# Kernel optimization log

Measured on AMD Instinct MI355X. Metric: run time of the kernel, lower is better.

The kernel has to match this reference:

```python
import jax, jax.numpy as jnp
import numpy as np

B, N, E, H, L, T, IN = 32, 512, 32768, 64, 2, 2, 8
TAU = 0.5


def setup_inputs() -> dict:
    key = jax.random.key(0)
    ks = jax.random.split(key, 32)
    f = lambda i, shape, s=0.05: jax.random.normal(ks[i], shape, jnp.float32) * s
    u = jax.random.uniform(ks[3], (B, E, T), jnp.float32, 1e-6, 1.0 - 1e-6)
    return {
        "inputs": f(0, (B, N, IN), 1.0),
        "hidden": f(1, (B, N, H), 1.0),
        "edge_logits": f(2, (B, E, T), 1.0),
        "gumbel": -jnp.log(-jnp.log(u)),  # standard Gumbel noise (deterministic here)
        "send_edges": jax.random.randint(ks[4], (E,), 0, N),
        "recv_edges": jax.random.randint(ks[5], (E,), 0, N),
        "W1": f(6, (L, T, H, 2 * H)), "b1": f(7, (L, T, H)),
        "W2": f(8, (L, T, H, H)), "b2": f(9, (L, T, H)),
        "Whr": f(10, (H, L * H)), "Whi": f(11, (H, L * H)), "Whh": f(12, (H, L * H)),
        "Wir": f(13, (H, IN)), "bir": f(14, (H,)),
        "Wii": f(15, (H, IN)), "bii": f(16, (H,)),
        "Win": f(17, (H, IN)), "bin_w": f(18, (H,)),
        "Wm1": f(19, (H, H)), "bm1": f(20, (H,)),
        "Wm2": f(21, (H, H)), "bm2": f(22, (H,)),
        "Wdf": f(23, (N, N * H), 0.005), "bdf": f(24, (N,)),
        "Wloc": f(25, (N, N * H), 0.005), "bloc": f(26, (N,)),
        "Wscale": f(27, (N, N * H), 0.005), "bscale": f(28, (N,)),
    }


def _lin(x, W, b):
    return jnp.einsum('...i,oi->...o', x, W) + b


def reference(inputs, hidden, edge_logits, gumbel, send_edges, recv_edges,
              W1, b1, W2, b2, Whr, Whi, Whh,
              Wir, bir, Wii, bii, Win, bin_w,
              Wm1, bm1, Wm2, bm2,
              Wdf, bdf, Wloc, bloc, Wscale, bscale):
    # hard gumbel-softmax (straight-through)
    y_soft = jax.nn.softmax((edge_logits + gumbel) / TAU, axis=-1)
    y_hard = jax.nn.one_hot(jnp.argmax(y_soft, axis=-1), T, dtype=y_soft.dtype)
    edges = jax.lax.stop_gradient(y_hard - y_soft) + y_soft  # [B,E,T]

    # normalized receiver degree (zeros -> 1), as in edge2node_mat / degree
    deg = jnp.zeros((N,), jnp.float32).at[recv_edges].add(1.0)
    deg = jnp.where(deg == 0, 1.0, deg)

    hidden_ = hidden
    aggs = []
    norm = float(T)  # skip_first_edge_type=False
    for k in range(L):
        pre = jnp.concatenate([hidden_[:, recv_edges], hidden_[:, send_edges]], axis=-1)  # [B,E,2H]
        all_msgs = jnp.zeros((B, E, H), pre.dtype)
        for t in range(T):  # per-edge-type tanh MLP (eval mode: dropout off)
            m = jnp.tanh(jnp.einsum('bef,hf->beh', pre, W1[k, t]) + b1[k, t])
            m = jnp.tanh(jnp.einsum('beh,gh->beg', m, W2[k, t]) + b2[k, t])
            all_msgs = all_msgs + m * edges[:, :, t:t + 1] / norm
        # scatter-mean onto receiver nodes (= normalized edge2node matmul)
        agg = jnp.zeros((B, N, H), all_msgs.dtype).at[:, recv_edges].add(all_msgs) / deg[None, :, None]
        hidden_ = agg
        aggs.append(agg)
    agg = jnp.concatenate(aggs, axis=-1)  # [B,N,L*H]

    r = jax.nn.sigmoid(_lin(inputs, Wir, bir) + jnp.einsum('bnf,of->bno', agg, Whr))
    i = jax.nn.sigmoid(_lin(inputs, Wii, bii) + jnp.einsum('bnf,of->bno', agg, Whi))
    n = jnp.tanh(_lin(inputs, Win, bin_w) + r * jnp.einsum('bnf,of->bno', agg, Whh))
    hidden_new = (1.0 - i) * n + i * hidden  # [B,N,H]

    pred = _lin(jax.nn.relu(_lin(hidden_new, Wm1, bm1)), Wm2, bm2)
    flat = pred.reshape(B, -1)  # [B, N*H]
    df = 2.0 + jax.nn.softplus(flat @ Wdf.T + bdf)      # StudentT domain maps
    loc = flat @ Wloc.T + bloc
    scale = jax.nn.softplus(flat @ Wscale.T + bscale)
    return df, loc, scale, hidden_new, edges
```

## Files before the change

### kernel.cpp

```cpp
#include <hip/hip_runtime.h>

#define B_  32
#define N_  512
#define E_  32768
#define H_  64
#define L_  2
#define T_  2
#define IN_ 8

typedef __attribute__((ext_vector_type(4))) float f32x4;
typedef __attribute__((ext_vector_type(8))) short bf16x8;
typedef __attribute__((ext_vector_type(4))) short s16x4;

__device__ __forceinline__ short f2bf(float f){
  unsigned u = __float_as_uint(f);
  u += 0x7FFFu + ((u >> 16) & 1u);
  return (short)(u >> 16);
}
__device__ __forceinline__ float bf2f(short s){
  return __uint_as_float(((unsigned)(unsigned short)s) << 16);
}
__device__ __forceinline__ bf16x8 pack8(f32x4 a, f32x4 b){
  bf16x8 r;
  r[0]=f2bf(a[0]); r[1]=f2bf(a[1]); r[2]=f2bf(a[2]); r[3]=f2bf(a[3]);
  r[4]=f2bf(b[0]); r[5]=f2bf(b[1]); r[6]=f2bf(b[2]); r[7]=f2bf(b[3]);
  return r;
}
__device__ __forceinline__ float fast_tanh(float x){
  float e = __expf(2.0f * x);
  return 1.0f - __fdividef(2.0f, e + 1.0f);
}
__device__ __forceinline__ float fast_sigm(float x){
  return __fdividef(1.0f, 1.0f + __expf(-x));
}
__device__ __forceinline__ float softplus_f(float x){
  return fmaxf(x, 0.0f) + log1pf(__expf(-fabsf(x)));
}

__global__ void k_edges(const float* __restrict__ logits, const float* __restrict__ gum,
                        float* __restrict__ edges_out, unsigned char* __restrict__ type_out){
  int i = blockIdx.x * 256 + threadIdx.x;
  if(i >= B_ * E_) return;
  float l0 = logits[2*i]   + gum[2*i];
  float l1 = logits[2*i+1] + gum[2*i+1];
  int t = (l1 > l0) ? 1 : 0;
  edges_out[2*i]   = t ? 0.f : 1.f;
  edges_out[2*i+1] = t ? 1.f : 0.f;
  type_out[i] = (unsigned char)t;
}

__global__ void k_hist(const int* __restrict__ recvE, int* __restrict__ hist){
  int e = blockIdx.x * 256 + threadIdx.x;
  if(e < E_) atomicAdd(&hist[recvE[e]], 1);
}
__global__ void k_scan(const int* __restrict__ hist, int* __restrict__ row_start,
                       float* __restrict__ deg){
  __shared__ int a[512], bbuf[512];
  int t = threadIdx.x;
  int h = hist[t];
  a[t] = h;
  __syncthreads();
  int* cur = a; int* nxt = bbuf;
  for(int off = 1; off < 512; off <<= 1){
    int v = cur[t] + (t >= off ? cur[t - off] : 0);
    nxt[t] = v;
    __syncthreads();
    int* tmp = cur; cur = nxt; nxt = tmp;
  }
  row_start[t] = cur[t] - h;
  if(t == 0) row_start[512] = E_;
  deg[t] = (h == 0) ? 1.0f : (float)h;
}

__global__ void k_hist2(const int* __restrict__ recvE, const unsigned char* __restrict__ typ,
                        int* __restrict__ n0){
  __shared__ int lh[512];
  int b = blockIdx.y, tid = threadIdx.x;
  lh[tid] = 0; lh[tid + 256] = 0;
  __syncthreads();
  int e0 = blockIdx.x * 2048;
  for(int k = 0; k < 8; ++k){
    int e = e0 + k*256 + tid;
    if(typ[(size_t)b*E_ + e] == 0) atomicAdd(&lh[recvE[e]], 1);
  }
  __syncthreads();
  if(lh[tid])       atomicAdd(&n0[b*512 + tid],       lh[tid]);
  if(lh[tid + 256]) atomicAdd(&n0[b*512 + tid + 256], lh[tid + 256]);
}
__global__ void k_scan2(const int* __restrict__ n0, const int* __restrict__ row_start,
                        int* __restrict__ stt){
  __shared__ int a[512], bbuf[512];
  __shared__ int tot;
  int b = blockIdx.x, t = threadIdx.x;
  int h = n0[b*512 + t];
  a[t] = h;
  __syncthreads();
  int* cur = a; int* nxt = bbuf;
  for(int off = 1; off < 512; off <<= 1){
    int v = cur[t] + (t >= off ? cur[t - off] : 0);
    nxt[t] = v;
    __syncthreads();
    int* tmp = cur; cur = nxt; nxt = tmp;
  }
  if(t == 511) tot = cur[511];
  __syncthreads();
  int excl = cur[t] - h;
  stt[(b*2    )*513 + t] = excl;
  stt[(b*2 + 1)*513 + t] = tot + row_start[t] - excl;
  if(t == 0){ stt[(b*2)*513 + 512] = tot; stt[(b*2+1)*513 + 512] = E_; }
}
__global__ void k_perm2(const int* __restrict__ recvE, const unsigned char* __restrict__ typ,
                        const int* __restrict__ stt, int* __restrict__ cur0,
                        int* __restrict__ cur1, unsigned short* __restrict__ perm2){
  int i = blockIdx.x * 256 + threadIdx.x;
  int b = i >> 15, e = i & (E_ - 1);
  int r = recvE[e];
  int pos;
  if(typ[i] == 0) pos = stt[(b*2  )*513 + r] + atomicAdd(&cur0[b*512 + r], 1);
  else            pos = stt[(b*2+1)*513 + r] + atomicAdd(&cur1[b*512 + r], 1);
  perm2[(size_t)b*E_ + pos] = (unsigned short)e;
}

__launch_bounds__(256, 2)
__global__ void k_prep(const float* __restrict__ hid,
                       const float* __restrict__ W1, const float* __restrict__ b1,
                       unsigned short* __restrict__ P, int layer){
  __shared__ __align__(16) short WT[256 * 64];
  __shared__ float bias[256];
  __shared__ float hidl[32 * 64];

  const int tid = threadIdx.x;
  const int b   = blockIdx.y;
  const int nbase = blockIdx.x * 32;
  const float* W1k = W1 + layer * (T_ * H_ * 2 * H_);

  {
    int col = tid, slot = col >> 6, h = col & 63;
    int t = slot & 1, prt = slot >> 1;
    const float* src = W1k + t*8192 + h*128 + prt*64;
#pragma unroll
    for(int u = 0; u < 8; ++u){
      bf16x8 v = pack8(*(const f32x4*)(src + u*8), *(const f32x4*)(src + u*8 + 4));
      int bo = col*128 + ((u*16) ^ ((col & 7) << 4));
      *(bf16x8*)((char*)WT + bo) = v;
    }
    bias[col] = (slot < 2) ? b1[layer*128 + t*64 + h] : 0.0f;
  }
  {
    const float* src = hid + ((size_t)b*N_ + nbase)*H_;
    ((f32x4*)hidl)[tid]       = ((const f32x4*)src)[tid];
    ((f32x4*)hidl)[tid + 256] = ((const f32x4*)src)[tid + 256];
  }
  __syncthreads();

  const int col = tid;
  for(int n = 0; n < 32; ++n){
    const float* hrow = hidl + n*64;
    float acc = bias[col];
#pragma unroll
    for(int u = 0; u < 8; ++u){
      int bo = col*128 + ((u*16) ^ ((col & 7) << 4));
      bf16x8 wv = *(const bf16x8*)((const char*)WT + bo);
#pragma unroll
      for(int i = 0; i < 8; ++i) acc += hrow[u*8 + i] * bf2f(wv[i]);
    }
    P[(((size_t)b*N_ + nbase + n) << 8) + col] = (unsigned short)f2bf(acc);
  }
}

__launch_bounds__(256, 6)
__global__ void k_msg(const unsigned short* __restrict__ P,
                      const float* __restrict__ W2, const float* __restrict__ b2,
                      const int* __restrict__ recvE, const int* __restrict__ sendE,
                      const unsigned short* __restrict__ perm2,
                      const int* __restrict__ stt, const float* __restrict__ deg,
                      float* __restrict__ agg, int layer){
  __shared__ __align__(16) short m1_lds[64 * 64];
  __shared__ float acc[8][64];
  __shared__ float b2_lds[128];
  __shared__ short rl_lds[64];

  const int tid  = threadIdx.x;
  const int w    = tid >> 6, lane = tid & 63;
  const int l15  = lane & 15, l4 = lane >> 4;
  const int b    = blockIdx.y;
  const int nodeBase = blockIdx.x * 8;

  const float* W2k = W2 + layer * (T_ * H_ * H_);

  if(tid < 128) b2_lds[tid] = b2[layer*128 + tid];
  acc[tid >> 6][tid & 63] = 0.0f;
  { int t2 = tid + 256; acc[t2 >> 6][t2 & 63] = 0.0f; }

  bf16x8 B2f[2][2];
#pragma unroll
  for(int t = 0; t < 2; ++t)
#pragma unroll
    for(int ks = 0; ks < 2; ++ks){
      const float* p = W2k + (t*64 + w*16 + l15)*64 + ks*32 + l4*8;
      B2f[t][ks] = pack8(*(const f32x4*)p, *(const f32x4*)(p+4));
    }

  const int gcol = w*16 + l15;
  const unsigned short* permB = perm2 + (size_t)b * E_;
  const int* sttB = stt + b*2*513;

#pragma unroll
  for(int seg = 0; seg < 2; ++seg){
    const int s0 = sttB[seg*513 + nodeBase];
    const int s1 = sttB[seg*513 + nodeBase + 8];
    const int ntiles = (s1 - s0 + 63) >> 6;
    for(int it = 0; it < ntiles; ++it){
      const int sbase = s0 + it*64;
      {
        int el = tid >> 2, part = tid & 3;
        int s = sbase + el;
        int h0 = part * 16;
        int bo0 = el*128 + ((h0*2)      ^ ((el & 7) << 4));
        int bo1 = el*128 + ((h0*2 + 16) ^ ((el & 7) << 4));
        if(s < s1){
          int eid = permB[s];
          int rv = recvE[eid], sd = sendE[eid];
          if(part == 0) rl_lds[el] = (short)(rv - nodeBase);
          const unsigned short* pr = P + (((size_t)b*N_ + rv) << 8) + seg*64 + h0;
          const unsigned short* ps = P + (((size_t)b*N_ + sd) << 8) + (2+seg)*64 + h0;
          bf16x8 r0 = *(const bf16x8*)pr,  r1 = *(const bf16x8*)(pr + 8);
          bf16x8 q0 = *(const bf16x8*)ps,  q1 = *(const bf16x8*)(ps + 8);
          bf16x8 o0, o1;
#pragma unroll
          for(int i = 0; i < 8; ++i){
            o0[i] = f2bf(fast_tanh(bf2f(r0[i]) + bf2f(q0[i])));
            o1[i] = f2bf(fast_tanh(bf2f(r1[i]) + bf2f(q1[i])));
          }
          *(bf16x8*)((char*)m1_lds + bo0) = o0;
          *(bf16x8*)((char*)m1_lds + bo1) = o1;
        }else{
          if(part == 0) rl_lds[el] = 255;
          bf16x8 z = {};
          *(bf16x8*)((char*)m1_lds + bo0) = z;
          *(bf16x8*)((char*)m1_lds + bo1) = z;
        }
      }
      __syncthreads();

      f32x4 C2[4];
      { float bv = b2_lds[seg*64 + gcol];
#pragma unroll
        for(int ef = 0; ef < 4; ++ef) C2[ef] = (f32x4){bv, bv, bv, bv}; }
#pragma unroll
      for(int ks = 0; ks < 2; ++ks){
#pragma unroll
        for(int ef = 0; ef < 4; ++ef){
          int e = ef*16 + l15;
          int byteoff = e*128 + (((ks*32 + l4*8)*2) ^ ((e & 7) << 4));
          bf16x8 A = *(const bf16x8*)((const char*)m1_lds + byteoff);
          C2[ef] = __builtin_amdgcn_mfma_f32_16x16x32_bf16(A, B2f[seg][ks], C2[ef], 0, 0, 0);
        }
      }
      {
        int prl = -1; float pend = 0.f;
#pragma unroll
        for(int ef = 0; ef < 4; ++ef){
          s16x4 rl4 = *(const s16x4*)&rl_lds[ef*16 + l4*4];
#pragma unroll
          for(int r = 0; r < 4; ++r){
            int rl = rl4[r];
            if(rl != prl){
              if(prl >= 0) atomicAdd(&acc[prl][gcol], pend);
              pend = 0.f;
              prl = (rl == 255) ? -1 : rl;
            }
            if(rl != 255) pend += fast_tanh(C2[ef][r]);
          }
        }
        if(prl >= 0) atomicAdd(&acc[prl][gcol], pend);
      }
      __syncthreads();
    }
  }

#pragma unroll
  for(int q = 0; q < 2; ++q){
    int idx = tid + q*256;
    int rl = idx >> 6, g = idx & 63;
    int node = nodeBase + rl;
    agg[(((size_t)b*N_ + node) << 6) + g] = acc[rl][g] * 0.5f / deg[node];
  }
}

__launch_bounds__(256, 2)
__global__ void k_gru(const float* __restrict__ x, const float* __restrict__ hid,
                      const float* __restrict__ agg0, const float* __restrict__ agg1,
                      const float* __restrict__ Whr, const float* __restrict__ Whi,
                      const float* __restrict__ Whh,
                      const float* __restrict__ Wir, const float* __restrict__ bir,
                      const float* __restrict__ Wii, const float* __restrict__ bii,
                      const float* __restrict__ Win, const float* __restrict__ binw,
                      float* __restrict__ hnew){
  __shared__ short WhrT[128*64], WhiT[128*64], WhhT[128*64];
  __shared__ float WxT[3][8*64];
  __shared__ float bias[3][64];
  __shared__ float agg_lds[4][128];

  int tid = threadIdx.x;
  for(int s = tid; s < 8192; s += 256){
    int g = s >> 7, f = s & 127;
    WhrT[f*64+g] = f2bf(Whr[s]);
    WhiT[f*64+g] = f2bf(Whi[s]);
    WhhT[f*64+g] = f2bf(Whh[s]);
  }
  for(int s = tid; s < 512; s += 256){
    int g = s >> 3, j = s & 7;
    WxT[0][j*64+g] = Wir[s]; WxT[1][j*64+g] = Wii[s]; WxT[2][j*64+g] = Win[s];
  }
  if(tid < 64){ bias[0][tid] = bir[tid]; bias[1][tid] = bii[tid]; bias[2][tid] = binw[tid]; }
  __syncthreads();

  int w = tid >> 6, lane = tid & 63;
  for(int j = 0; j < 8; ++j){
    int id = blockIdx.x*32 + j*4 + w;
    size_t base = (size_t)id * 64;
    agg_lds[w][lane]      = agg0[base + lane];
    agg_lds[w][64 + lane] = agg1[base + lane];

    float ar = bias[0][lane], ai = bias[1][lane], an = bias[2][lane], ah = 0.f;
    const float* xp = x + (size_t)id * 8;
#pragma unroll
    for(int jj = 0; jj < 8; ++jj){
      float xv = xp[jj];
      ar += xv * WxT[0][jj*64+lane];
      ai += xv * WxT[1][jj*64+lane];
      an += xv * WxT[2][jj*64+lane];
    }
#pragma unroll 4
    for(int f = 0; f < 128; ++f){
      float av = agg_lds[w][f];
      ar += av * bf2f(WhrT[f*64+lane]);
      ai += av * bf2f(WhiT[f*64+lane]);
      ah += av * bf2f(WhhT[f*64+lane]);
    }
    float r  = fast_sigm(ar);
    float ii = fast_sigm(ai);
    float ng = fast_tanh(an + r * ah);
    float ho = hid[base + lane];
    hnew[base + lane] = (1.0f - ii) * ng + ii * ho;
  }
}

__launch_bounds__(256, 2)
__global__ void k_pred(const float* __restrict__ hnew,
                       const float* __restrict__ Wm1, const float* __restrict__ bm1,
                       const float* __restrict__ Wm2, const float* __restrict__ bm2,
                       float* __restrict__ flat){
  __shared__ float W1T[64*64], W2T[64*64];
  __shared__ float bias1[64], bias2[64];
  __shared__ float h_lds[4][64], t_lds[4][64];
  int tid = threadIdx.x;
  for(int s = tid; s < 4096; s += 256){
    int g = s >> 6, h = s & 63;
    W1T[h*64+g] = Wm1[s];
    W2T[h*64+g] = Wm2[s];
  }
  if(tid < 64){ bias1[tid] = bm1[tid]; bias2[tid] = bm2[tid]; }
  __syncthreads();

  int w = tid >> 6, lane = tid & 63;
  for(int j = 0; j < 8; ++j){
    int id = blockIdx.x*32 + j*4 + w;
    size_t base = (size_t)id * 64;
    h_lds[w][lane] = hnew[base + lane];
    float a = bias1[lane];
#pragma unroll 4
    for(int h = 0; h < 64; ++h) a += h_lds[w][h] * W1T[h*64+lane];
    a = fmaxf(a, 0.0f);
    t_lds[w][lane] = a;
    float p = bias2[lane];
#pragma unroll 4
    for(int h = 0; h < 64; ++h) p += t_lds[w][h] * W2T[h*64+lane];
    flat[base + lane] = p;
  }
}

__launch_bounds__(512, 2)
__global__ void k_out(const float* __restrict__ flat,
                      const float* __restrict__ Wdf,  const float* __restrict__ bdf,
                      const float* __restrict__ Wloc, const float* __restrict__ bloc,
                      const float* __restrict__ Wsc,  const float* __restrict__ bsc,
                      float* __restrict__ out){
  __shared__ float red[512 * 32];
  int tid = threadIdx.x;
  int mat = blockIdx.y;
  int o0  = blockIdx.x * 4;
  const float* W    = (mat == 0) ? Wdf  : (mat == 1) ? Wloc : Wsc;
  const float* bias = (mat == 0) ? bdf  : (mat == 1) ? bloc : bsc;
  int jj = tid & 127, bc = tid >> 7;
  float acc[4][8] = {};
  for(int jc = 0; jc < 64; ++jc){
    int j = jc*512 + jj*4;
    f32x4 wv[4];
#pragma unroll
    for(int o = 0; o < 4; ++o) wv[o] = *(const f32x4*)(W + (size_t)(o0+o)*32768 + j);
#pragma unroll
    for(int u = 0; u < 8; ++u){
      int bb = bc*8 + u;
      f32x4 fv = *(const f32x4*)(flat + (size_t)bb*32768 + j);
#pragma unroll
      for(int o = 0; o < 4; ++o)
        acc[o][u] += fv[0]*wv[o][0] + fv[1]*wv[o][1] + fv[2]*wv[o][2] + fv[3]*wv[o][3];
    }
  }
#pragma unroll
  for(int o = 0; o < 4; ++o)
#pragma unroll
    for(int u = 0; u < 8; ++u)
      red[tid*32 + ((o*8+u) ^ (tid & 31))] = acc[o][u];
  __syncthreads();
  if(tid < 128){
    int bcf = tid >> 5, v = tid & 31, o = v >> 3, u = v & 7;
    float s = 0.f;
    for(int q = 0; q < 128; ++q){
      int t = bcf*128 + q;
      s += red[t*32 + (v ^ (t & 31))];
    }
    int bb = bcf*8 + u, og = o0 + o;
    s += bias[og];
    float res = (mat == 0) ? 2.0f + softplus_f(s) : (mat == 1) ? s : softplus_f(s);
    out[(size_t)mat*16384 + (size_t)bb*512 + og] = res;
  }
}

extern "C" void kernel_launch(void* const* d_in, const int* in_sizes, int n_in,
                              void* d_out, int out_size, void* d_ws, size_t ws_size,
                              hipStream_t stream){
  (void)in_sizes; (void)n_in; (void)out_size; (void)ws_size;
  const float* inputs = (const float*)d_in[0];
  const float* hidden = (const float*)d_in[1];
  const float* elog   = (const float*)d_in[2];
  const float* gum    = (const float*)d_in[3];
  const int*   sendE  = (const int*)  d_in[4];
  const int*   recvE  = (const int*)  d_in[5];
  const float* W1   = (const float*)d_in[6];
  const float* b1   = (const float*)d_in[7];
  const float* W2   = (const float*)d_in[8];
  const float* b2   = (const float*)d_in[9];
  const float* Whr  = (const float*)d_in[10];
  const float* Whi  = (const float*)d_in[11];
  const float* Whh  = (const float*)d_in[12];
  const float* Wir  = (const float*)d_in[13]; const float* bir  = (const float*)d_in[14];
  const float* Wii  = (const float*)d_in[15]; const float* bii  = (const float*)d_in[16];
  const float* Win  = (const float*)d_in[17]; const float* binw = (const float*)d_in[18];
  const float* Wm1  = (const float*)d_in[19]; const float* bm1  = (const float*)d_in[20];
  const float* Wm2  = (const float*)d_in[21]; const float* bm2  = (const float*)d_in[22];
  const float* Wdf  = (const float*)d_in[23]; const float* bdf  = (const float*)d_in[24];
  const float* Wloc = (const float*)d_in[25]; const float* bloc = (const float*)d_in[26];
  const float* Wsc  = (const float*)d_in[27]; const float* bsc  = (const float*)d_in[28];

  float* out       = (float*)d_out;
  float* out_hid   = out + 49152;
  float* out_edges = out + 1097728;

  char* ws = (char*)d_ws;
  float* agg0 = (float*)(ws);
  float* agg1 = (float*)(ws + 4194304);
  unsigned short* P = (unsigned short*)(ws + 8388608);
  float* flat = (float*)(ws + 8388608);
  unsigned short* perm2 = (unsigned short*)(ws + 16777216);
  unsigned char* typ = (unsigned char*)(ws + 18874368);
  int*   hist      = (int*)(ws + 19922944);
  int*   row_start = (int*)(ws + 19924992);
  float* deg       = (float*)(ws + 19929088);
  int*   n0        = (int*)(ws + 19931136);
  int*   cur0      = (int*)(ws + 19996672);
  int*   cur1      = (int*)(ws + 20062208);
  int*   stt       = (int*)(ws + 20127744);

  hipMemsetAsync(hist, 0, 2048, stream);
  hipMemsetAsync(n0, 0, 3*65536, stream);

  k_edges<<<4096, 256, 0, stream>>>(elog, gum, out_edges, typ);
  k_hist<<<128, 256, 0, stream>>>(recvE, hist);
  k_scan<<<1, 512, 0, stream>>>(hist, row_start, deg);
  k_hist2<<<dim3(16, 32), 256, 0, stream>>>(recvE, typ, n0);
  k_scan2<<<32, 512, 0, stream>>>(n0, row_start, stt);
  k_perm2<<<4096, 256, 0, stream>>>(recvE, typ, stt, cur0, cur1, perm2);

  k_prep<<<dim3(16, 32), 256, 0, stream>>>(hidden, W1, b1, P, 0);
  k_msg<<<dim3(64, 32), 256, 0, stream>>>(P, W2, b2, recvE, sendE,
                                          perm2, stt, deg, agg0, 0);
  k_prep<<<dim3(16, 32), 256, 0, stream>>>(agg0, W1, b1, P, 1);
  k_msg<<<dim3(64, 32), 256, 0, stream>>>(P, W2, b2, recvE, sendE,
                                          perm2, stt, deg, agg1, 1);

  k_gru<<<512, 256, 0, stream>>>(inputs, hidden, agg0, agg1,
                                 Whr, Whi, Whh, Wir, bir, Wii, bii, Win, binw, out_hid);
  k_pred<<<512, 256, 0, stream>>>(out_hid, Wm1, bm1, Wm2, bm2, flat);
  k_out<<<dim3(128, 3), 512, 0, stream>>>(flat, Wdf, bdf, Wloc, bloc, Wsc, bsc, out);
}
```

Baseline: 581.0 us.

## Compute output projections with bf16 MFMA, split-K atomics, and bf16 flat activations

k_pred now writes the flattened prediction as bf16. The final three 512x32768 projections use MFMA 16x16x32 bf16 tiles with a 32-way split-K, accumulate into a zeroed buffer with atomics, and a separate finalize kernel adds bias and applies softplus. This is meant to replace the scalar FMA GEMV-like kernel, which was bound by the bandwidth of reading the fp32 weights, with matrix-core compute and more parallelism. It adds bf16 rounding of weights and activations, a memset plus an extra kernel launch, and nondeterministic atomic summation order.

```diff
diff --git a/kernel.cpp b/kernel.cpp
--- a/kernel.cpp
+++ b/kernel.cpp
@@ -351,7 +351,7 @@
 __global__ void k_pred(const float* __restrict__ hnew,
                        const float* __restrict__ Wm1, const float* __restrict__ bm1,
                        const float* __restrict__ Wm2, const float* __restrict__ bm2,
-                       float* __restrict__ flat){
+                       unsigned short* __restrict__ flatbf){
   __shared__ float W1T[64*64], W2T[64*64];
   __shared__ float bias1[64], bias2[64];
   __shared__ float h_lds[4][64], t_lds[4][64];
@@ -377,56 +377,58 @@
     float p = bias2[lane];
 #pragma unroll 4
     for(int h = 0; h < 64; ++h) p += t_lds[w][h] * W2T[h*64+lane];
-    flat[base + lane] = p;
-  }
-}
-
-__launch_bounds__(512, 2)
-__global__ void k_out(const float* __restrict__ flat,
-                      const float* __restrict__ Wdf,  const float* __restrict__ bdf,
-                      const float* __restrict__ Wloc, const float* __restrict__ bloc,
-                      const float* __restrict__ Wsc,  const float* __restrict__ bsc,
-                      float* __restrict__ out){
-  __shared__ float red[512 * 32];
-  int tid = threadIdx.x;
-  int mat = blockIdx.y;
-  int o0  = blockIdx.x * 4;
-  const float* W    = (mat == 0) ? Wdf  : (mat == 1) ? Wloc : Wsc;
-  const float* bias = (mat == 0) ? bdf  : (mat == 1) ? bloc : bsc;
-  int jj = tid & 127, bc = tid >> 7;
-  float acc[4][8] = {};
-  for(int jc = 0; jc < 64; ++jc){
-    int j = jc*512 + jj*4;
-    f32x4 wv[4];
-#pragma unroll
-    for(int o = 0; o < 4; ++o) wv[o] = *(const f32x4*)(W + (size_t)(o0+o)*32768 + j);
-#pragma unroll
-    for(int u = 0; u < 8; ++u){
-      int bb = bc*8 + u;
-      f32x4 fv = *(const f32x4*)(flat + (size_t)bb*32768 + j);
-#pragma unroll
-      for(int o = 0; o < 4; ++o)
-        acc[o][u] += fv[0]*wv[o][0] + fv[1]*wv[o][1] + fv[2]*wv[o][2] + fv[3]*wv[o][3];
-    }
-  }
-#pragma unroll
-  for(int o = 0; o < 4; ++o)
-#pragma unroll
-    for(int u = 0; u < 8; ++u)
-      red[tid*32 + ((o*8+u) ^ (tid & 31))] = acc[o][u];
-  __syncthreads();
-  if(tid < 128){
-    int bcf = tid >> 5, v = tid & 31, o = v >> 3, u = v & 7;
-    float s = 0.f;
-    for(int q = 0; q < 128; ++q){
-      int t = bcf*128 + q;
-      s += red[t*32 + (v ^ (t & 31))];
-    }
-    int bb = bcf*8 + u, og = o0 + o;
-    s += bias[og];
-    float res = (mat == 0) ? 2.0f + softplus_f(s) : (mat == 1) ? s : softplus_f(s);
-    out[(size_t)mat*16384 + (size_t)bb*512 + og] = res;
-  }
+    flatbf[base + lane] = (unsigned short)f2bf(p);
+  }
+}
+
+__launch_bounds__(256, 6)
+__global__ void k_out(const float* __restrict__ Wdf, const float* __restrict__ Wloc,
+                      const float* __restrict__ Wsc,
+                      const unsigned short* __restrict__ flatbf,
+                      float* __restrict__ pacc){
+  const int bid = blockIdx.x;
+  const int mt  = bid >> 5;
+  const int kb  = bid & 31;
+  const int row0 = mt * 32;
+  const int mat  = row0 >> 9;
+  const int rloc = row0 & 511;
+  const float* W = (mat == 0) ? Wdf : (mat == 1) ? Wloc : Wsc;
+
+  const int tid = threadIdx.x, w = tid >> 6, lane = tid & 63;
+  const int l15 = lane & 15, l4 = lane >> 4;
+  const float* wp = W + (size_t)(rloc + (w & 1)*16 + l15)*32768 + kb*1024 + l4*8;
+  const unsigned short* fp = flatbf + (size_t)((w >> 1)*16 + l15)*32768 + kb*1024 + l4*8;
+
+  f32x4 acc0 = {}, acc1 = {};
+#pragma unroll 4
+  for(int ks = 0; ks < 32; ks += 2){
+    f32x4 a0 = *(const f32x4*)(wp + ks*32);
+    f32x4 a1 = *(const f32x4*)(wp + ks*32 + 4);
+    bf16x8 Bv0 = *(const bf16x8*)(fp + ks*32);
+    f32x4 a2 = *(const f32x4*)(wp + ks*32 + 32);
+    f32x4 a3 = *(const f32x4*)(wp + ks*32 + 36);
+    bf16x8 Bv1 = *(const bf16x8*)(fp + ks*32 + 32);
+    acc0 = __builtin_amdgcn_mfma_f32_16x16x32_bf16(pack8(a0, a1), Bv0, acc0, 0, 0, 0);
+    acc1 = __builtin_amdgcn_mfma_f32_16x16x32_bf16(pack8(a2, a3), Bv1, acc1, 0, 0, 0);
+  }
+#pragma unroll
+  for(int r = 0; r < 4; ++r){
+    int grow = row0 + (w & 1)*16 + l4*4 + r;
+    atomicAdd(&pacc[grow*32 + (w >> 1)*16 + l15], acc0[r] + acc1[r]);
+  }
+}
+
+__global__ void k_fin(const float* __restrict__ pacc,
+                      const float* __restrict__ bdf, const float* __restrict__ bloc,
+                      const float* __restrict__ bsc, float* __restrict__ out){
+  int i = blockIdx.x*256 + threadIdx.x;
+  int mat = i >> 14;
+  int rem = i & 16383;
+  int b = rem >> 9, og = rem & 511;
+  float s = pacc[(mat*512 + og)*32 + b];
+  s += (mat == 0 ? bdf : mat == 1 ? bloc : bsc)[og];
+  float res = (mat == 0) ? 2.0f + softplus_f(s) : (mat == 1) ? s : softplus_f(s);
+  out[i] = res;
 }
 
 extern "C" void kernel_launch(void* const* d_in, const int* in_sizes, int n_in,
@@ -463,7 +465,7 @@
   float* agg0 = (float*)(ws);
   float* agg1 = (float*)(ws + 4194304);
   unsigned short* P = (unsigned short*)(ws + 8388608);
-  float* flat = (float*)(ws + 8388608);
+  unsigned short* flatbf = (unsigned short*)(ws + 8388608);
   unsigned short* perm2 = (unsigned short*)(ws + 16777216);
   unsigned char* typ = (unsigned char*)(ws + 18874368);
   int*   hist      = (int*)(ws + 19922944);
@@ -473,6 +475,7 @@
   int*   cur0      = (int*)(ws + 19996672);
   int*   cur1      = (int*)(ws + 20062208);
   int*   stt       = (int*)(ws + 20127744);
+  float* pacc      = agg0;
 
   hipMemsetAsync(hist, 0, 2048, stream);
   hipMemsetAsync(n0, 0, 3*65536, stream);
@@ -493,6 +496,8 @@
 
   k_gru<<<512, 256, 0, stream>>>(inputs, hidden, agg0, agg1,
                                  Whr, Whi, Whh, Wir, bir, Wii, bii, Win, binw, out_hid);
-  k_pred<<<512, 256, 0, stream>>>(out_hid, Wm1, bm1, Wm2, bm2, flat);
-  k_out<<<dim3(128, 3), 512, 0, stream>>>(flat, Wdf, bdf, Wloc, bloc, Wsc, bsc, out);
-}
+  k_pred<<<512, 256, 0, stream>>>(out_hid, Wm1, bm1, Wm2, bm2, flatbf);
+  hipMemsetAsync(pacc, 0, 1536*32*4, stream);
+  k_out<<<1536, 256, 0, stream>>>(Wdf, Wloc, Wsc, flatbf, pacc);
+  k_fin<<<192, 256, 0, stream>>>(pacc, bdf, bloc, bsc, out);
+}
```

After: 523.5 us. 1.11x faster.
